# Performance work log

Measured on AMD Instinct MI355X. Metric: run time of the kernel, lower is better.

Reference implementation:

```python
import jax, jax.numpy as jnp
import numpy as np

DIM = 1024; VOCAB = 32000; HEADS = 16; HEAD_DIM = DIM // HEADS
SEG = 128; NPT = 16; WIDTH = 128
THETA = 0.1; ETA = 0.9; ALPHA = 0.01; EPS = 1e-6  # neural-memory lr / momentum / weight-decay


def l2n(x):
    return x / (jnp.linalg.norm(x, axis=-1, keepdims=True) + EPS)


def mlp(p, x):
    # 2-layer memory MLP: dim -> width -> dim, SiLU
    W1, b1, W2, b2 = p
    return jax.nn.silu(x @ W1 + b1) @ W2 + b2


def setup_inputs() -> dict:
    key = jax.random.key(0)
    ks = jax.random.split(key, 12)
    g = lambda k, s: jax.random.normal(k, s, jnp.float32) * 0.02
    z = lambda n: jnp.zeros((n,), jnp.float32)
    return {
        "x": jax.random.randint(ks[0], (2, 512), 0, VOCAB),
        "embedding": g(ks[1], (VOCAB, DIM)),
        "persistent": g(ks[2], (NPT, DIM)),
        "Wq": g(ks[3], (DIM, DIM)), "bq": z(DIM),
        "Wk": g(ks[4], (DIM, DIM)), "bk": z(DIM),
        "Wv": g(ks[5], (DIM, DIM)), "bv": z(DIM),
        "attn_in_w": g(ks[6], (DIM, 3 * DIM)), "attn_in_b": z(3 * DIM),
        "attn_out_w": g(ks[7], (DIM, DIM)), "attn_out_b": z(DIM),
        "mW1": g(ks[8], (DIM, WIDTH)), "mb1": z(WIDTH),
        "mW2": g(ks[9], (WIDTH, DIM)), "mb2": z(DIM),
        "head_w": g(ks[10], (DIM, VOCAB)), "head_b": z(VOCAB),
    }


def reference(x, embedding, persistent, Wq, bq, Wk, bk, Wv, bv,
              attn_in_w, attn_in_b, attn_out_w, attn_out_b,
              mW1, mb1, mW2, mb2, head_w, head_b):
    B, N = x.shape
    x_emb = embedding[x]  # [B, N, D]
    pad = (-N) % SEG
    if pad:
        x_emb = jnp.pad(x_emb, ((0, 0), (0, pad), (0, 0)))
    S = x_emb.shape[1] // SEG
    segs = x_emb.reshape(B, S, SEG, DIM).transpose(1, 0, 2, 3)  # [S, B, L, D]

    T = NPT + 2 * SEG  # persistent + retrieved memory + segment tokens
    causal = jnp.triu(jnp.ones((T, T), bool), 1)

    def mha(xc):  # [B, T, D] -> [B, T, D], torch nn.MultiheadAttention math
        q, k, v = jnp.split(xc @ attn_in_w + attn_in_b, 3, axis=-1)
        split = lambda t: t.reshape(B, T, HEADS, HEAD_DIM).transpose(0, 2, 1, 3)
        q, k, v = split(q), split(k), split(v)
        scores = jnp.einsum('bhqd,bhkd->bhqk', q, k) / np.sqrt(HEAD_DIM).astype(np.float32)
        scores = jnp.where(causal, -jnp.inf, scores)
        out = jnp.einsum('bhqk,bhkd->bhqd', jax.nn.softmax(scores, axis=-1), v)
        return out.transpose(0, 2, 1, 3).reshape(B, T, DIM) @ attn_out_w + attn_out_b

    # per-sample memory params (leading B axis) + zero momentum
    params0 = tuple(jnp.broadcast_to(w, (B,) + w.shape) for w in (mW1, mb1, mW2, mb2))
    mom0 = tuple(jnp.zeros_like(p) for p in params0)

    def mem_loss(p, k, v):
        e = mlp(p, k) - v
        return jnp.sum(e * e)

    def tok_step(carry, tok):  # tok: [B, D] -- one test-time gradient step on memory
        p, m = carry
        k = jax.lax.stop_gradient(l2n(tok @ Wk + bk))  # stop_grad_k=True
        v = tok @ Wv + bv                               # stop_grad_v=False
        grads = jax.vmap(jax.grad(mem_loss))(p, k, v)
        m = jax.tree.map(lambda mm, g: ETA * mm - THETA * g, m, grads)
        p = jax.tree.map(lambda pp, mm: (1.0 - ALPHA) * pp + mm, p, m)
        return (p, m), None

    retrieve = jax.vmap(mlp)  # vmap over per-sample memory params

    def seg_step(carry, segment):  # segment: [B, L, D]
        p, m = carry
        h = retrieve(p, l2n(segment @ Wq + bq))
        combined = jnp.concatenate(
            [jnp.broadcast_to(persistent, (B, NPT, DIM)), h, segment], axis=1)
        seg_out = mha(combined)[:, -SEG:, :]
        (p, m), _ = jax.lax.scan(tok_step, (p, m), seg_out.transpose(1, 0, 2))
        mem_out = retrieve(p, l2n(seg_out @ Wq + bq))
        return (p, m), seg_out * mem_out

    _, outs = jax.lax.scan(seg_step, (params0, mom0), segs)  # outs: [S, B, L, D]
    full = outs.transpose(1, 0, 2, 3).reshape(B, S * SEG, DIM)[:, :N, :]
    return full @ head_w + head_b
```

## Files before the change

### kernel.cpp

```cpp
#include <hip/hip_runtime.h>
#include <math.h>

#define D_    1024
#define B_    2
#define N_    512
#define SEG_  128
#define NSEG_ 4
#define NPT_  16
#define T_    272
#define NH_   16
#define HD_   64
#define W_    128
#define V_    32000

#define THETA_ 0.1f
#define ETA_   0.9f
#define PDEC_  0.99f
#define EPSN_  1e-6f
#define NB2_  32
#define FSTR_ 32

typedef __bf16 bf16x8 __attribute__((ext_vector_type(8)));
typedef float  f32x4  __attribute__((ext_vector_type(4)));

static const size_t XEMB = 0;
static const size_t OUTS = XEMB + (size_t)B_*N_*D_;
static const size_t PW1  = OUTS + (size_t)B_*N_*D_;
static const size_t PB1  = PW1  + (size_t)B_*D_*W_;
static const size_t PW2T = PB1  + (size_t)B_*W_;
static const size_t PB2  = PW2T + (size_t)B_*D_*W_;
static const size_t MOM  = PB2  + (size_t)B_*D_;
static const size_t MW1  = MOM;
static const size_t MB1  = MW1  + (size_t)B_*D_*W_;
static const size_t MW2T = MB1  + (size_t)B_*W_;
static const size_t MB2  = MW2T + (size_t)B_*D_*W_;
static const size_t MOMSZ = (size_t)B_*(D_*W_ + W_ + D_*W_ + D_);
static const size_t Q1   = MOM  + MOMSZ;
static const size_t AH   = Q1   + (size_t)B_*SEG_*D_;
static const size_t HBUF = AH   + (size_t)B_*SEG_*W_;
static const size_t COMB = HBUF + (size_t)B_*SEG_*D_;
static const size_t QKV  = COMB + (size_t)B_*T_*D_;
static const size_t ATTN = QKV  + (size_t)B_*T_*3*D_;
static const size_t SEGO = ATTN + (size_t)B_*SEG_*D_;
static const size_t KM   = SEGO + (size_t)B_*SEG_*D_;
static const size_t VM   = KM   + (size_t)B_*SEG_*D_;
static const size_t MEMO = VM   + (size_t)B_*SEG_*D_;
static const size_t WSEND = MEMO + (size_t)B_*SEG_*D_;

static const size_t AQ1K  = QKV;
static const size_t AQ1KM = AQ1K  + 32768;
static const size_t AGRAM = AQ1KM + 32768;
static const size_t ADZ1  = AGRAM + 32768;
static const size_t AA1H  = ADZ1  + 32768;
static const size_t AEH   = AA1H  + 32768;
static const size_t AEXR  = AEH + (size_t)B_*SEG_*D_;
static const size_t AEXEE = AEXR + 16384;
static const size_t COEF  = WSEND;
static const size_t ZEROB = COEF + 512;
static const size_t CBAR  = ZEROB + 128;

__device__ __forceinline__ float sigf(float x) { return 1.f/(1.f+expf(-x)); }

__device__ __forceinline__ void gstore(float* p, float v) {
  __hip_atomic_store(p, v, __ATOMIC_RELAXED, __HIP_MEMORY_SCOPE_AGENT);
}
__device__ __forceinline__ float gload(const float* p) {
  return __hip_atomic_load(p, __ATOMIC_RELAXED, __HIP_MEMORY_SCOPE_AGENT);
}

__device__ __forceinline__ void bsplit(float a, short& h, short& l) {
  unsigned u = __builtin_bit_cast(unsigned, a);
  unsigned hb = (u + 0x7fffu + ((u >> 16) & 1u)) >> 16;
  h = (short)hb;
  float hf = __builtin_bit_cast(float, hb << 16);
  float r = a - hf;
  unsigned ur = __builtin_bit_cast(unsigned, r);
  unsigned lb = (ur + 0x7fffu + ((ur >> 16) & 1u)) >> 16;
  l = (short)lb;
}

template<int BT, int SILU>
__global__ __launch_bounds__(256) void k_gemm(
    const float* __restrict__ A, const float* __restrict__ Bm,
    const float* __restrict__ bias, float* __restrict__ C,
    int M, int N, int K, long sA, long sB, long sC, long sBias)
{
  __shared__ float As[16][68];
  __shared__ float Bs[16][68];
  int bz = blockIdx.z;
  A += bz*sA; Bm += bz*sB; C += bz*sC; bias += bz*sBias;
  int n0 = blockIdx.x*64, m0 = blockIdx.y*64;
  int tid = threadIdx.x;
  int tx = tid & 15, ty = tid >> 4;
  int r  = tid >> 2;
  int kq = (tid & 3) * 4;
  float acc[4][4] = {};
  for (int k0 = 0; k0 < K; k0 += 16) {
    {
      int row = m0 + r;
      float4 v = make_float4(0.f,0.f,0.f,0.f);
      if (row < M) v = *(const float4*)(A + (long)row*K + k0 + kq);
      As[kq+0][r]=v.x; As[kq+1][r]=v.y; As[kq+2][r]=v.z; As[kq+3][r]=v.w;
    }
    if (BT) {
      int row = n0 + r;
      float4 v = *(const float4*)(Bm + (long)row*K + k0 + kq);
      Bs[kq+0][r]=v.x; Bs[kq+1][r]=v.y; Bs[kq+2][r]=v.z; Bs[kq+3][r]=v.w;
    } else {
      int c = tid & 63, r4 = tid >> 6;
      #pragma unroll
      for (int p = 0; p < 4; p++) {
        int kk = r4 + p*4;
        Bs[kk][c] = Bm[(long)(k0+kk)*N + n0 + c];
      }
    }
    __syncthreads();
    #pragma unroll
    for (int kk = 0; kk < 16; kk++) {
      float av[4], bv[4];
      #pragma unroll
      for (int i=0;i<4;i++) av[i] = As[kk][ty*4+i];
      #pragma unroll
      for (int j=0;j<4;j++) bv[j] = Bs[kk][tx*4+j];
      #pragma unroll
      for (int i=0;i<4;i++)
        #pragma unroll
        for (int j=0;j<4;j++)
          acc[i][j] = fmaf(av[i], bv[j], acc[i][j]);
    }
    __syncthreads();
  }
  #pragma unroll
  for (int i=0;i<4;i++) {
    int row = m0 + ty*4 + i;
    if (row >= M) continue;
    #pragma unroll
    for (int j=0;j<4;j++) {
      int col = n0 + tx*4 + j;
      float v = acc[i][j] + bias[col];
      if (SILU) v = v * sigf(v);
      C[(long)row*N + col] = v;
    }
  }
}

__global__ __launch_bounds__(256) void k_gemm2(
    const float* __restrict__ A, const float* __restrict__ B1,
    const float* __restrict__ B2, float* __restrict__ C1, float* __restrict__ C2,
    int K, long sA, long sB, long sC)
{
  __shared__ float As[16][68];
  __shared__ float B1s[16][68];
  __shared__ float B2s[16][68];
  int bz = blockIdx.z;
  A += bz*sA; B1 += bz*sB; B2 += bz*sB; C1 += bz*sC; C2 += bz*sC;
  int n0 = blockIdx.x*64, m0 = blockIdx.y*64;
  int tid = threadIdx.x;
  int tx = tid & 15, ty = tid >> 4;
  int r  = tid >> 2;
  int kq = (tid & 3) * 4;
  float acc1[4][4] = {}, acc2[4][4] = {};
  for (int k0 = 0; k0 < K; k0 += 16) {
    {
      float4 v = *(const float4*)(A + (long)(m0+r)*K + k0 + kq);
      As[kq+0][r]=v.x; As[kq+1][r]=v.y; As[kq+2][r]=v.z; As[kq+3][r]=v.w;
    }
    {
      int c = tid & 63, r4 = tid >> 6;
      #pragma unroll
      for (int p = 0; p < 4; p++) {
        int kk = r4 + p*4;
        B1s[kk][c] = B1[(long)(k0+kk)*W_ + n0 + c];
        B2s[kk][c] = B2[(long)(k0+kk)*W_ + n0 + c];
      }
    }
    __syncthreads();
    #pragma unroll
    for (int kk = 0; kk < 16; kk++) {
      float av[4], b1v[4], b2v[4];
      #pragma unroll
      for (int i=0;i<4;i++) av[i] = As[kk][ty*4+i];
      #pragma unroll
      for (int j=0;j<4;j++) { b1v[j] = B1s[kk][tx*4+j]; b2v[j] = B2s[kk][tx*4+j]; }
      #pragma unroll
      for (int i=0;i<4;i++)
        #pragma unroll
        for (int j=0;j<4;j++) {
          acc1[i][j] = fmaf(av[i], b1v[j], acc1[i][j]);
          acc2[i][j] = fmaf(av[i], b2v[j], acc2[i][j]);
        }
    }
    __syncthreads();
  }
  #pragma unroll
  for (int i=0;i<4;i++) {
    int row = m0 + ty*4 + i;
    #pragma unroll
    for (int j=0;j<4;j++) {
      int col = n0 + tx*4 + j;
      C1[(long)row*W_ + col] = acc1[i][j];
      C2[(long)row*W_ + col] = acc2[i][j];
    }
  }
}

__global__ __launch_bounds__(256) void k_gemm_mfma(
    const float* __restrict__ A, const float* __restrict__ Bm,
    const float* __restrict__ bias, float* __restrict__ C,
    int M, int N, int K, long sA, long sB, long sC, long sBias)
{
  __shared__ short Ah[128][48];
  __shared__ short Al[128][48];
  __shared__ short Bh[32][132];
  __shared__ short Bl[32][132];
  int bz = blockIdx.z;
  A += bz*sA; Bm += bz*sB; C += bz*sC; bias += bz*sBias;
  int n0 = blockIdx.x*128, m0 = blockIdx.y*128;
  int tid = threadIdx.x;
  int wave = tid >> 6, lane = tid & 63;
  int wm = (wave >> 1) * 64, wn = (wave & 1) * 64;
  int lrow = lane & 15, lk = (lane >> 4) * 8;
  int arow0 = min(m0 + (tid >> 1), M-1);
  f32x4 acc[4][4] = {};
  for (int k0 = 0; k0 < K; k0 += 32) {
    __syncthreads();
    {
      int r = tid >> 1, kq = (tid & 1) * 16;
      const float* ap = A + (long)arow0*K + k0 + kq;
      #pragma unroll
      for (int q = 0; q < 16; q += 4) {
        float4 v = *(const float4*)(ap + q);
        short h0,l0,h1,l1,h2,l2,h3,l3;
        bsplit(v.x,h0,l0); bsplit(v.y,h1,l1); bsplit(v.z,h2,l2); bsplit(v.w,h3,l3);
        *(short4*)&Ah[r][kq+q] = make_short4(h0,h1,h2,h3);
        *(short4*)&Al[r][kq+q] = make_short4(l0,l1,l2,l3);
      }
    }
    {
      int kr = tid >> 3, nq = (tid & 7) * 16;
      const float* bp = Bm + (long)(k0 + kr)*N + n0 + nq;
      #pragma unroll
      for (int q = 0; q < 16; q += 4) {
        float4 v = *(const float4*)(bp + q);
        short h0,l0,h1,l1,h2,l2,h3,l3;
        bsplit(v.x,h0,l0); bsplit(v.y,h1,l1); bsplit(v.z,h2,l2); bsplit(v.w,h3,l3);
        *(short4*)&Bh[kr][nq+q] = make_short4(h0,h1,h2,h3);
        *(short4*)&Bl[kr][nq+q] = make_short4(l0,l1,l2,l3);
      }
    }
    __syncthreads();
    bf16x8 bh[4], bl[4];
    #pragma unroll
    for (int nf = 0; nf < 4; nf++) {
      int col = wn + nf*16 + lrow;
      #pragma unroll
      for (int j = 0; j < 8; j++) {
        bh[nf][j] = __builtin_bit_cast(__bf16, Bh[lk+j][col]);
        bl[nf][j] = __builtin_bit_cast(__bf16, Bl[lk+j][col]);
      }
    }
    #pragma unroll
    for (int mf = 0; mf < 4; mf++) {
      int ar2 = wm + mf*16 + lrow;
      bf16x8 ah = *(const bf16x8*)&Ah[ar2][lk];
      bf16x8 al = *(const bf16x8*)&Al[ar2][lk];
      #pragma unroll
      for (int nf = 0; nf < 4; nf++) {
        acc[mf][nf] = __builtin_amdgcn_mfma_f32_16x16x32_bf16(ah, bh[nf], acc[mf][nf], 0, 0, 0);
        acc[mf][nf] = __builtin_amdgcn_mfma_f32_16x16x32_bf16(ah, bl[nf], acc[mf][nf], 0, 0, 0);
        acc[mf][nf] = __builtin_amdgcn_mfma_f32_16x16x32_bf16(al, bh[nf], acc[mf][nf], 0, 0, 0);
      }
    }
  }
  #pragma unroll
  for (int mf = 0; mf < 4; mf++) {
    #pragma unroll
    for (int nf = 0; nf < 4; nf++) {
      int col = n0 + wn + nf*16 + lrow;
      float bv = bias[col];
      #pragma unroll
      for (int j = 0; j < 4; j++) {
        int row = m0 + wm + mf*16 + (lane >> 4)*4 + j;
        if (row < M) C[(long)row*N + col] = acc[mf][nf][j] + bv;
      }
    }
  }
}

__global__ __launch_bounds__(256) void k_qkv_mfma(
    const float* __restrict__ pers, const float* __restrict__ hbuf,
    const float* __restrict__ xemb, int s,
    const float* __restrict__ Bm, const float* __restrict__ bias,
    float* __restrict__ C)
{
  __shared__ short Ah[128][48];
  __shared__ short Al[128][48];
  __shared__ short Bh[32][132];
  __shared__ short Bl[32][132];
  const int M = B_*T_, N = 3*D_, K = D_;
  int n0 = blockIdx.x*128, m0 = blockIdx.y*128;
  int tid = threadIdx.x;
  int wave = tid >> 6, lane = tid & 63;
  int wm = (wave >> 1) * 64, wn = (wave & 1) * 64;
  int lrow = lane & 15, lk = (lane >> 4) * 8;
  int grow = min(m0 + (tid >> 1), M-1);
  int b = grow >= T_ ? 1 : 0;
  int rt = grow - b*T_;
  const float* asrc;
  if (rt < NPT_)            asrc = pers + (long)rt*D_;
  else if (rt < NPT_+SEG_)  asrc = hbuf + ((long)b*SEG_ + (rt-NPT_))*D_;
  else                      asrc = xemb + ((long)b*N_ + s*SEG_ + (rt-NPT_-SEG_))*D_;
  f32x4 acc[4][4] = {};
  for (int k0 = 0; k0 < K; k0 += 32) {
    __syncthreads();
    {
      int r = tid >> 1, kq = (tid & 1) * 16;
      const float* ap = asrc + k0 + kq;
      #pragma unroll
      for (int q = 0; q < 16; q += 4) {
        float4 v = *(const float4*)(ap + q);
        short h0,l0,h1,l1,h2,l2,h3,l3;
        bsplit(v.x,h0,l0); bsplit(v.y,h1,l1); bsplit(v.z,h2,l2); bsplit(v.w,h3,l3);
        *(short4*)&Ah[r][kq+q] = make_short4(h0,h1,h2,h3);
        *(short4*)&Al[r][kq+q] = make_short4(l0,l1,l2,l3);
      }
    }
    {
      int kr = tid >> 3, nq = (tid & 7) * 16;
      const float* bp = Bm + (long)(k0 + kr)*N + n0 + nq;
      #pragma unroll
      for (int q = 0; q < 16; q += 4) {
        float4 v = *(const float4*)(bp + q);
        short h0,l0,h1,l1,h2,l2,h3,l3;
        bsplit(v.x,h0,l0); bsplit(v.y,h1,l1); bsplit(v.z,h2,l2); bsplit(v.w,h3,l3);
        *(short4*)&Bh[kr][nq+q] = make_short4(h0,h1,h2,h3);
        *(short4*)&Bl[kr][nq+q] = make_short4(l0,l1,l2,l3);
      }
    }
    __syncthreads();
    bf16x8 bh[4], bl[4];
    #pragma unroll
    for (int nf = 0; nf < 4; nf++) {
      int col = wn + nf*16 + lrow;
      #pragma unroll
      for (int j = 0; j < 8; j++) {
        bh[nf][j] = __builtin_bit_cast(__bf16, Bh[lk+j][col]);
        bl[nf][j] = __builtin_bit_cast(__bf16, Bl[lk+j][col]);
      }
    }
    #pragma unroll
    for (int mf = 0; mf < 4; mf++) {
      int ar2 = wm + mf*16 + lrow;
      bf16x8 ah = *(const bf16x8*)&Ah[ar2][lk];
      bf16x8 al = *(const bf16x8*)&Al[ar2][lk];
      #pragma unroll
      for (int nf = 0; nf < 4; nf++) {
        acc[mf][nf] = __builtin_amdgcn_mfma_f32_16x16x32_bf16(ah, bh[nf], acc[mf][nf], 0, 0, 0);
        acc[mf][nf] = __builtin_amdgcn_mfma_f32_16x16x32_bf16(ah, bl[nf], acc[mf][nf], 0, 0, 0);
        acc[mf][nf] = __builtin_amdgcn_mfma_f32_16x16x32_bf16(al, bh[nf], acc[mf][nf], 0, 0, 0);
      }
    }
  }
  #pragma unroll
  for (int mf = 0; mf < 4; mf++) {
    #pragma unroll
    for (int nf = 0; nf < 4; nf++) {
      int col = n0 + wn + nf*16 + lrow;
// ... 155 lines not shown
      #pragma unroll
      for (int nf = 0; nf < 4; nf++) {
        acc[mf][nf] = __builtin_amdgcn_mfma_f32_16x16x32_bf16(ah, bh[nf], acc[mf][nf], 0, 0, 0);
        acc[mf][nf] = __builtin_amdgcn_mfma_f32_16x16x32_bf16(ah, bl[nf], acc[mf][nf], 0, 0, 0);
        acc[mf][nf] = __builtin_amdgcn_mfma_f32_16x16x32_bf16(al, bh[nf], acc[mf][nf], 0, 0, 0);
      }
    }
  }
  #pragma unroll
  for (int mf = 0; mf < 4; mf++) {
    #pragma unroll
    for (int nf = 0; nf < 4; nf++) {
      int col = n0 + wn + nf*16 + lrow;
      float bv = bias[col];
      #pragma unroll
      for (int j = 0; j < 4; j++) {
        int row = m0 + wm + mf*16 + (lane >> 4)*4 + j;
        C[(long)row*N + col] = acc[mf][nf][j] + bv;
      }
    }
  }
}

__global__ void k_embed(const int* __restrict__ x, const float* __restrict__ emb,
                        float* __restrict__ xe)
{
  int row = blockIdx.x, tid = threadIdx.x;
  int idx = x[row];
  float4 v = *(const float4*)(emb + (long)idx*D_ + tid*4);
  *(float4*)(xe + (long)row*D_ + tid*4) = v;
}

#define PER_ 263296L
__global__ void k_init(const float* __restrict__ mW1in, const float* __restrict__ mb1in,
                       const float* __restrict__ mW2in, const float* __restrict__ mb2in,
                       float* __restrict__ pW1, float* __restrict__ pb1,
                       float* __restrict__ pW2T, float* __restrict__ pb2)
{
  long g = (long)blockIdx.x*256 + threadIdx.x;
  if (g >= 2*PER_) return;
  int b = (int)(g / PER_);
  long rr = g % PER_;
  if (rr < 131072)       pW1[(long)b*131072 + rr] = mW1in[rr];
  else if (rr < 131200)  pb1[b*W_ + (rr-131072)] = mb1in[rr-131072];
  else if (rr < 262272) { long l = rr-131200; int j=(int)(l>>7), h=(int)(l&127);
                          pW2T[(long)b*131072 + l] = mW2in[(long)h*D_ + j]; }
  else                   pb2[b*D_ + (rr-262272)] = mb2in[rr-262272];
}

__global__ void k_coef(float* __restrict__ c)
{
  if (blockIdx.x == 0 && threadIdx.x == 0) {
    c[0] = 1.f; c[128] = 1.f;
    float A = 1.f, eta_d = 1.f;
    for (int d = 1; d < 128; d++) {
      eta_d *= ETA_;
      A = PDEC_*A + eta_d;
      c[d] = A;
      c[128 + d] = eta_d;
    }
    c[256] = 1.f;
    float bp = 1.f;
    for (int t = 1; t <= 128; t++) { bp *= PDEC_; c[256 + t] = bp; }
  }
}

__global__ __launch_bounds__(256) void k_l2n(float* __restrict__ X)
{
  long row = blockIdx.x;
  float* p = X + row*D_;
  int tid = threadIdx.x;
  float4 v = *(float4*)(p + tid*4);
  float ss = v.x*v.x + v.y*v.y + v.z*v.z + v.w*v.w;
  for (int o=32;o;o>>=1) ss += __shfl_xor(ss,o);
  __shared__ float wsum[4];
  if ((tid&63)==0) wsum[tid>>6] = ss;
  __syncthreads();
  float tot = wsum[0]+wsum[1]+wsum[2]+wsum[3];
  float sc = 1.f/(sqrtf(tot)+EPSN_);
  v.x*=sc; v.y*=sc; v.z*=sc; v.w*=sc;
  *(float4*)(p + tid*4) = v;
}

__global__ __launch_bounds__(256) void k_attn(const float* __restrict__ qkv,
                                              float* __restrict__ outp)
{
  __shared__ float sQ[16][68];
  __shared__ float sKV[64][68];
  __shared__ float sS[16][273];
  int qt = blockIdx.x, head = blockIdx.y, b = blockIdx.z;
  int tid = threadIdx.x;
  const float* base = qkv + (long)b*T_*3*D_;
  int qoff = head*HD_, koff = D_ + head*HD_, voff = 2*D_ + head*HD_;
  int qrow0 = NPT_ + SEG_ + qt*16;
  {
    int rr = tid>>4, c4 = (tid&15)*4;
    float4 v = *(const float4*)(base + (long)(qrow0+rr)*3*D_ + qoff + c4);
    sQ[rr][c4]=v.x; sQ[rr][c4+1]=v.y; sQ[rr][c4+2]=v.z; sQ[rr][c4+3]=v.w;
  }
  __syncthreads();
  for (int j0 = 0; j0 < T_; j0 += 64) {
    int chunk = min(64, T_ - j0);
    {
      int jj = tid>>2, cq = (tid&3)*16;
      if (jj < chunk) {
        #pragma unroll
        for (int q4=0;q4<4;q4++) {
          float4 v = *(const float4*)(base + (long)(j0+jj)*3*D_ + koff + cq + q4*4);
          sKV[jj][cq+q4*4]=v.x; sKV[jj][cq+q4*4+1]=v.y; sKV[jj][cq+q4*4+2]=v.z; sKV[jj][cq+q4*4+3]=v.w;
        }
      }
    }
    __syncthreads();
    int rr = tid>>4, jj0 = tid&15;
    #pragma unroll
    for (int p=0;p<4;p++) {
      int jj = jj0 + p*16;
      if (jj < chunk) {
        float s = 0.f;
        #pragma unroll 8
        for (int c=0;c<HD_;c++) s = fmaf(sQ[rr][c], sKV[jj][c], s);
        s *= 0.125f;
        int jg = j0 + jj, qg = qrow0 + rr;
        if (jg > qg) s = -3.0e38f;
        sS[rr][jg] = s;
      }
    }
    __syncthreads();
  }
  {
    int rr = tid>>4, l16 = tid&15;
    float m = -3.4e38f;
    for (int j=l16; j<T_; j+=16) m = fmaxf(m, sS[rr][j]);
    for (int o=8;o;o>>=1) m = fmaxf(m, __shfl_xor(m,o));
    float sum = 0.f;
    for (int j=l16; j<T_; j+=16) { float e = expf(sS[rr][j]-m); sS[rr][j] = e; sum += e; }
    for (int o=8;o;o>>=1) sum += __shfl_xor(sum,o);
    float inv = 1.f/sum;
    for (int j=l16; j<T_; j+=16) sS[rr][j] *= inv;
  }
  __syncthreads();
  float acc[4] = {0.f,0.f,0.f,0.f};
  int rr = tid>>4, c4 = (tid&15)*4;
  for (int j0 = 0; j0 < T_; j0 += 64) {
    int chunk = min(64, T_ - j0);
    {
      int jj = tid>>2, cq = (tid&3)*16;
      if (jj < chunk) {
        #pragma unroll
        for (int q4=0;q4<4;q4++) {
          float4 v = *(const float4*)(base + (long)(j0+jj)*3*D_ + voff + cq + q4*4);
          sKV[jj][cq+q4*4]=v.x; sKV[jj][cq+q4*4+1]=v.y; sKV[jj][cq+q4*4+2]=v.z; sKV[jj][cq+q4*4+3]=v.w;
        }
      }
    }
    __syncthreads();
    for (int jj=0; jj<chunk; jj++) {
      float p = sS[rr][j0+jj];
      #pragma unroll
      for (int i=0;i<4;i++) acc[i] = fmaf(p, sKV[jj][c4+i], acc[i]);
    }
    __syncthreads();
  }
  float4 o4 = make_float4(acc[0],acc[1],acc[2],acc[3]);
  *(float4*)(outp + ((long)(b*SEG_) + qt*16 + rr)*D_ + head*HD_ + c4) = o4;
}

__device__ __forceinline__ void gbar(int* flags, int blk, int gen)
{
  asm volatile("s_waitcnt vmcnt(0) lgkmcnt(0)" ::: "memory");
  __syncthreads();
  if (threadIdx.x == 0)
    __hip_atomic_store(flags + blk*FSTR_, gen, __ATOMIC_RELAXED, __HIP_MEMORY_SCOPE_AGENT);
  if (threadIdx.x < NB2_) {
    while (__hip_atomic_load(flags + threadIdx.x*FSTR_, __ATOMIC_RELAXED,
                             __HIP_MEMORY_SCOPE_AGENT) < gen)
      __builtin_amdgcn_s_sleep(1);
  }
  __syncthreads();
}

__global__ __launch_bounds__(256) void k_scan(
  const float* __restrict__ pW2T, const float* __restrict__ mW2T,
  float* __restrict__ pb1, float* __restrict__ mb1,
  float* __restrict__ pb2, float* __restrict__ mb2,
  const float* __restrict__ Vm,
  const float* __restrict__ q1k, const float* __restrict__ q1km,
  const float* __restrict__ G,
  float* __restrict__ dz1o, float* __restrict__ a1o, float* __restrict__ eo,
  float* __restrict__ exR, float* __restrict__ exEE,
  const float* __restrict__ coef, int* __restrict__ barbase, int seg)
{
  __shared__ float sDZ[128][129];
  __shared__ float sA1[128][129];
  __shared__ float sEh[128][33];
  __shared__ float sB1[128], sMB1[128], sZ1[128], sR[128];
  __shared__ float sB2[32], sMB2[32];
  __shared__ float sAt[128];
  __shared__ float sBp[129];
  __shared__ float sGc[128];
  __shared__ float sS[128];
  __shared__ float sEEc[128];
  __shared__ float sP[2][128];

  int b = blockIdx.y, blk = blockIdx.x, tid = threadIdx.x;
  int j0 = blk*32;
  int* flags = barbase + b*(NB2_*FSTR_);
  int gbase = seg*200;
  const float* W0 = pW2T + (long)b*131072;
  const float* Wm = mW2T + (long)b*131072;

  int jD = tid >> 3, lD = tid & 7;
  float rD0[16], rDm[16];
  #pragma unroll
  for (int k = 0; k < 16; k++) {
    rD0[k] = W0[(long)(j0+jD)*128 + lD + 8*k];
    rDm[k] = Wm[(long)(j0+jD)*128 + lD + 8*k];
  }
  int hE = tid >> 1, halfE = tid & 1;
  float rE0[16], rEm[16];
  #pragma unroll
  for (int q = 0; q < 16; q++) {
    rE0[q] = W0[(long)(j0 + halfE*16 + q)*128 + hE];
    rEm[q] = Wm[(long)(j0 + halfE*16 + q)*128 + hE];
  }

  int hB = tid & 127, halfB = tid >> 7;
  if (tid < 128) { sAt[tid] = coef[tid]; sB1[tid] = pb1[b*W_+tid]; sMB1[tid] = mb1[b*W_+tid]; }
  else if (tid < 160) { int j = tid-128; sB2[j] = pb2[b*D_+j0+j]; sMB2[j] = mb2[b*D_+j0+j]; }
  for (int i = tid; i < 129; i += 256) sBp[i] = coef[256+i];
  __syncthreads();

  for (int t = 0; t < SEG_; ++t) {
    int par = t & 1;
    float bp = sBp[t];
    float ca = (t>0) ? ETA_*sAt[t-1] : 0.f;
    int th = t >> 1;

    float rq1k = 0.f, rq1km = 0.f;
    if (tid < 128) {
      rq1k  = q1k [((long)b*SEG_+t)*W_ + tid];
      rq1km = q1km[((long)b*SEG_+t)*W_ + tid];
      if (t > 0) {
        float mm = ETA_*sMB1[tid] - THETA_*sDZ[t-1][tid];
        sMB1[tid] = mm; sB1[tid] = PDEC_*sB1[tid] + mm;
      }
      if (tid < t) sGc[tid] = sAt[t-1-tid]*G[((long)b*SEG_+t)*SEG_ + tid];
    } else if (tid < 160) {
      int j = tid-128;
      if (t > 0) {
        float mm = ETA_*sMB2[j] - 2.f*THETA_*sEh[t-1][j];
        sMB2[j] = mm; sB2[j] = PDEC_*sB2[j] + mm;
      }
    }
    __syncthreads();

    {
      int u0 = halfB ? th : 0, u1 = halfB ? t : th;
      float acc = 0.f;
      for (int u = u0; u < u1; ++u) acc = fmaf(sGc[u], sDZ[u][hB], acc);
      sP[halfB][hB] = acc;
    }
    __syncthreads();
    if (tid < 128) {
      float z1 = bp*rq1k + ca*rq1km + sB1[tid] - THETA_*(sP[0][tid] + sP[1][tid]);
      sZ1[tid] = z1;
      sA1[t][tid] = z1 * sigf(z1);
    }
    __syncthreads();

    {
      int u = tid & 127, half = tid >> 7;
      float acc = 0.f;
      if (u < t) {
        #pragma unroll 8
        for (int h = half*64; h < half*64 + 64; ++h)
          acc = fmaf(sA1[u][h], sA1[t][h], acc);
      }
      sP[half][u] = acc;
    }
    __syncthreads();
    if (tid < t) sS[tid] = -2.f*THETA_*sAt[t-1-tid]*(sP[0][tid] + sP[1][tid]);
    __syncthreads();

    {
      float g = 0.f, gm = 0.f;
      #pragma unroll
      for (int k = 0; k < 16; k++) {
        float a = sA1[t][lD + 8*k];
        g  = fmaf(rD0[k], a, g);
        gm = fmaf(rDm[k], a, gm);
      }
      float corr = 0.f;
      for (int u = lD; u < t; u += 8) corr = fmaf(sS[u], sEh[u][jD], corr);
      float tot = bp*g + ca*gm + corr;
      tot += __shfl_xor(tot,4); tot += __shfl_xor(tot,2); tot += __shfl_xor(tot,1);
      if (lD == 0) sEh[t][jD] = tot + sB2[jD] - Vm[((long)b*SEG_+t)*D_ + j0+jD];
    }
    __syncthreads();

    {
      float racc = 0.f;
      #pragma unroll
      for (int q = 0; q < 16; ++q) {
        float w = bp*rE0[q] + ca*rEm[q];
        racc = fmaf(w, sEh[t][halfE*16 + q], racc);
      }
      racc += __shfl_xor(racc,1);
      if (halfE == 0) gstore(&exR[(((long)par*B_ + b)*NB2_ + blk)*W_ + hE], racc);
      if (hE < t) {
        float eacc = 0.f;
        #pragma unroll
        for (int q = 0; q < 16; ++q)
          eacc = fmaf(sEh[hE][halfE*16 + q], sEh[t][halfE*16 + q], eacc);
        eacc += __shfl_xor(eacc,1);
        if (halfE == 0) gstore(&exEE[(((long)par*B_ + b)*NB2_ + blk)*W_ + hE], eacc);
      }
    }
    gbar(flags, blk, gbase + t + 1);

    {
      float racc = 0.f;
      #pragma unroll
      for (int k = 0; k < 16; ++k)
        racc += gload(&exR[(((long)par*B_ + b)*NB2_ + halfE*16 + k)*W_ + hE]);
      racc += __shfl_xor(racc,1);
      if (halfE == 0) sR[hE] = racc;
      if (hE < t) {
        float eacc = 0.f;
        #pragma unroll
        for (int k = 0; k < 16; ++k)
          eacc += gload(&exEE[(((long)par*B_ + b)*NB2_ + halfE*16 + k)*W_ + hE]);
        eacc += __shfl_xor(eacc,1);
        if (halfE == 0) sEEc[hE] = -2.f*THETA_*sAt[t-1-hE]*eacc;
      }
    }
    __syncthreads();
    {
      int u0 = halfB ? th : 0, u1 = halfB ? t : th;
      float acc = 0.f;
      for (int u = u0; u < u1; ++u) acc = fmaf(sEEc[u], sA1[u][hB], acc);
      sP[halfB][hB] = acc;
    }
    __syncthreads();
    if (tid < 128) {
      float macc = sP[0][tid] + sP[1][tid];
      float z = sZ1[tid], sg = sigf(z);
      sDZ[t][tid] = 2.f*(sR[tid] + macc)*sg*(1.f + z*(1.f - sg));
    }
    __syncthreads();
  }

  if (tid < 128) {
    if (blk == 0) {
      float mm = ETA_*sMB1[tid] - THETA_*sDZ[127][tid];
      mb1[b*W_ + tid] = mm;
      pb1[b*W_ + tid] = PDEC_*sB1[tid] + mm;
    }
  } else if (tid < 160) {
    int j = tid-128;
    float mm = ETA_*sMB2[j] - 2.f*THETA_*sEh[127][j];
    mb2[b*D_ + j0+j] = mm;
    pb2[b*D_ + j0+j] = PDEC_*sB2[j] + mm;
  }
  for (int i = tid; i < 128*4; i += 256) {
    int t2 = i >> 2, hh = (i & 3) + blk*4;
    dz1o[((long)b*SEG_+t2)*W_ + hh] = sDZ[t2][hh];
    a1o [((long)b*SEG_+t2)*W_ + hh] = sA1[t2][hh];
  }
  for (int i = tid; i < 128*32; i += 256) {
    int t2 = i >> 5, jj = i & 31;
    eo[((long)b*SEG_+t2)*D_ + j0+jj] = sEh[t2][jj];
  }
}

__global__ __launch_bounds__(256) void k_recon(
  float* __restrict__ pW1, float* __restrict__ mW1,
  float* __restrict__ pW2T, float* __restrict__ mW2T,
  const float* __restrict__ KMp, const float* __restrict__ Eh,
  const float* __restrict__ DZ1, const float* __restrict__ A1h,
  const float* __restrict__ coef)
{
  __shared__ float s1[16][33];
  __shared__ float s2[16][65];
  __shared__ float sCA[128], sCE[128];
  int dt = blockIdx.x, ht = blockIdx.y, kb = blockIdx.z;
  int kind = kb >> 1, b = kb & 1;
  int tid = threadIdx.x;
  int d0 = dt*32, hb = ht*64;
  const float* in1 = (kind ? Eh : KMp) + (long)b*SEG_*D_;
  const float* in2 = (kind ? A1h : DZ1) + (long)b*SEG_*W_;
  float* Pb = (kind ? pW2T : pW1) + (long)b*131072;
  float* Mb = (kind ? mW2T : mW1) + (long)b*131072;
  float f = kind ? -2.f*THETA_ : -THETA_;
  if (tid < 128) {
    sCA[tid] = f*coef[127 - tid];
    sCE[tid] = f*coef[128 + 127 - tid];
  }
  __syncthreads();
  int dd = tid >> 3, le = tid & 7;
  float accP[8] = {}, accM[8] = {};
  for (int u0 = 0; u0 < 128; u0 += 16) {
    for (int i = tid; i < 16*32; i += 256) {
      int uu = i >> 5, d2 = i & 31;
      s1[uu][d2] = in1[(long)(u0+uu)*D_ + d0 + d2];
    }
    for (int i = tid; i < 16*64; i += 256) {
      int uu = i >> 6, hl = i & 63;
      s2[uu][hl] = in2[(long)(u0+uu)*W_ + hb + hl];
    }
    __syncthreads();
    #pragma unroll
    for (int uu = 0; uu < 16; uu++) {
      float a = s1[uu][dd];
      float cAu = sCA[u0+uu], cEu = sCE[u0+uu];
      #pragma unroll
      for (int k = 0; k < 8; k++) {
        float v = a * s2[uu][k*8 + le];
        accP[k] = fmaf(cAu, v, accP[k]);
        accM[k] = fmaf(cEu, v, accM[k]);
      }
    }
    __syncthreads();
  }
  float b128 = coef[256 + 128];
  float eA   = ETA_*coef[127];
  float e128 = ETA_*coef[128 + 127];
  #pragma unroll
  for (int k = 0; k < 8; k++) {
    long idx = (long)(d0+dd)*W_ + hb + k*8 + le;
    float Po = Pb[idx], Mo = Mb[idx];
    Pb[idx] = b128*Po + eA*Mo + accP[k];
    Mb[idx] = e128*Mo + accM[k];
  }
}

__global__ void k_mul(const float* __restrict__ so, const float* __restrict__ mo,
                      float* __restrict__ outs, int s)
{
  int l = blockIdx.x, b = blockIdx.y, tid = threadIdx.x;
  long src = ((long)b*SEG_ + l)*D_ + tid*4;
  float4 a = *(const float4*)(so + src);
  float4 c = *(const float4*)(mo + src);
  a.x*=c.x; a.y*=c.y; a.z*=c.z; a.w*=c.w;
  *(float4*)(outs + ((long)b*N_ + s*SEG_ + l)*D_ + tid*4) = a;
}

static inline void gemm(const float* A, const float* Bm, const float* bias, float* C,
                        int M, int N, int K, long sA, long sB, long sC, long sBias,
                        int batch, int bt, int silu_, hipStream_t st)
{
  dim3 g(N/64, (M+63)/64, batch), blk(256);
  if (!bt && !silu_) k_gemm<0,0><<<g,blk,0,st>>>(A,Bm,bias,C,M,N,K,sA,sB,sC,sBias);
  else if (!bt && silu_) k_gemm<0,1><<<g,blk,0,st>>>(A,Bm,bias,C,M,N,K,sA,sB,sC,sBias);
  else k_gemm<1,0><<<g,blk,0,st>>>(A,Bm,bias,C,M,N,K,sA,sB,sC,sBias);
}

extern "C" void kernel_launch(void* const* d_in, const int* in_sizes, int n_in,
                              void* d_out, int out_size, void* d_ws, size_t ws_size,
                              hipStream_t stream)
{
  (void)in_sizes; (void)n_in; (void)out_size; (void)ws_size;
  const int*   x     = (const int*)  d_in[0];
  const float* emb   = (const float*)d_in[1];
  const float* pers  = (const float*)d_in[2];
  const float* Wq    = (const float*)d_in[3];
  const float* bq    = (const float*)d_in[4];
  const float* Wk    = (const float*)d_in[5];
  const float* bk    = (const float*)d_in[6];
  const float* Wv    = (const float*)d_in[7];
  const float* bv    = (const float*)d_in[8];
  const float* aiw   = (const float*)d_in[9];
  const float* aib   = (const float*)d_in[10];
  const float* aow   = (const float*)d_in[11];
  const float* aob   = (const float*)d_in[12];
  const float* mW1in = (const float*)d_in[13];
  const float* mb1in = (const float*)d_in[14];
  const float* mW2in = (const float*)d_in[15];
  const float* mb2in = (const float*)d_in[16];
  const float* headw = (const float*)d_in[17];
  const float* headb = (const float*)d_in[18];
  float* out = (float*)d_out;
  float* ws  = (float*)d_ws;

  hipMemsetAsync(ws + MOM, 0, MOMSZ*sizeof(float), stream);
  hipMemsetAsync(ws + ZEROB, 0, 128*sizeof(float), stream);
  hipMemsetAsync(ws + CBAR, 0, (size_t)B_*NB2_*FSTR_*sizeof(int), stream);
  k_embed<<<dim3(B_*N_), dim3(256), 0, stream>>>(x, emb, ws+XEMB);
  k_init<<<dim3((2*PER_+255)/256), dim3(256), 0, stream>>>(
      mW1in, mb1in, mW2in, mb2in, ws+PW1, ws+PB1, ws+PW2T, ws+PB2);
  k_coef<<<dim3(1), dim3(64), 0, stream>>>(ws+COEF);

  for (int s = 0; s < NSEG_; s++) {
    const float* segA = ws + XEMB + (size_t)s*SEG_*D_;
    k_gemm_mfma<<<dim3(8, 1, B_), dim3(256), 0, stream>>>(
        segA, Wq, bq, ws+Q1, SEG_, D_, D_, (long)N_*D_, 0, (long)SEG_*D_, 0);
    k_l2n<<<dim3(B_*SEG_), dim3(256), 0, stream>>>(ws+Q1);
    gemm(ws+Q1, ws+PW1, ws+PB1, ws+AH, SEG_, W_, D_, (long)SEG_*D_, (long)D_*W_, (long)SEG_*W_, W_, B_, 0, 1, stream);
    gemm(ws+AH, ws+PW2T, ws+PB2, ws+HBUF, SEG_, D_, W_, (long)SEG_*W_, (long)D_*W_, (long)SEG_*D_, D_, B_, 1, 0, stream);
    k_qkv_mfma<<<dim3(3*D_/128, (B_*T_+127)/128), dim3(256), 0, stream>>>(
        pers, ws+HBUF, ws+XEMB, s, aiw, aib, ws+QKV);
    k_attn<<<dim3(8, NH_, B_), dim3(256), 0, stream>>>(ws+QKV, ws+ATTN);
    k_gemm_mfma<<<dim3(D_/128, 2, 1), dim3(256), 0, stream>>>(
        ws+ATTN, aow, aob, ws+SEGO, B_*SEG_, D_, D_, 0, 0, 0, 0);
    k_gemmkvq_m<<<dim3(24, 2), dim3(256), 0, stream>>>(
        ws+SEGO, Wk, bk, Wv, bv, Wq, bq, ws+KM, ws+VM, ws+Q1);
    k_l2n<<<dim3(B_*SEG_), dim3(256), 0, stream>>>(ws+KM);
    k_l2n<<<dim3(B_*SEG_), dim3(256), 0, stream>>>(ws+Q1);
    k_gemm2<<<dim3(2, 2, B_), dim3(256), 0, stream>>>(
        ws+KM, ws+PW1, ws+MW1, ws+AQ1K, ws+AQ1KM,
        D_, (long)SEG_*D_, (long)D_*W_, (long)SEG_*W_);
    gemm(ws+KM, ws+KM,  ws+ZEROB, ws+AGRAM, SEG_, SEG_, D_, (long)SEG_*D_, (long)SEG_*D_, (long)SEG_*SEG_, 0, B_, 1, 0, stream);
    k_scan<<<dim3(NB2_, B_), dim3(256), 0, stream>>>(
        ws+PW2T, ws+MW2T, ws+PB1, ws+MB1, ws+PB2, ws+MB2, ws+VM,
        ws+AQ1K, ws+AQ1KM, ws+AGRAM,
        ws+ADZ1, ws+AA1H, ws+AEH,
        ws+AEXR, ws+AEXEE,
        ws+COEF, (int*)(ws+CBAR), s);
    k_recon<<<dim3(32, 2, 4), dim3(256), 0, stream>>>(
        ws+PW1, ws+MW1, ws+PW2T, ws+MW2T,
        ws+KM, ws+AEH, ws+ADZ1, ws+AA1H, ws+COEF);
    gemm(ws+Q1, ws+PW1, ws+PB1, ws+AH, SEG_, W_, D_, (long)SEG_*D_, (long)D_*W_, (long)SEG_*W_, W_, B_, 0, 1, stream);
    gemm(ws+AH, ws+PW2T, ws+PB2, ws+MEMO, SEG_, D_, W_, (long)SEG_*W_, (long)D_*W_, (long)SEG_*D_, D_, B_, 1, 0, stream);
    k_mul<<<dim3(SEG_, B_), dim3(256), 0, stream>>>(ws+SEGO, ws+MEMO, ws+OUTS, s);
  }
  k_head_mfma<<<dim3(V_/128, (B_*N_)/128), dim3(256), 0, stream>>>(
      ws+OUTS, headw, headb, out, B_*N_, V_, D_);
}
```

Measured before the change: 7.650 ms.

## Replace scalar FP32 memory-MLP GEMMs with split-bf16 MFMA kernel and fuse epilogues

Replaces the scalar 64x64-tile FP32 GEMM used for the memory MLP retrieval and the key Gram matrix with a templated split-bf16 MFMA kernel (128x128 tiles), adding SiLU and optional elementwise-multiply epilogues. The final retrieval GEMM now multiplies by the segment output and writes straight into the output buffer, which removes the separate k_mul kernel. The two l2-normalisations are merged into one launch. The scan kernel's two-half partial sums are also collapsed back into single-thread loops, which removes a sync per step but halves the parallelism of those reductions. The small GEMMs now launch as few as two blocks, and precision depends on the hi/lo bf16 split.

Result: no change. 7.678 ms (+0.4%).

```diff
diff --git a/kernel.cpp b/kernel.cpp
--- a/kernel.cpp
+++ b/kernel.cpp
@@ -79,67 +79,104 @@
   l = (short)lb;
 }
 
-template<int BT, int SILU>
-__global__ __launch_bounds__(256) void k_gemm(
+template<int BT, int SILU, int MUL>
+__global__ __launch_bounds__(256) void k_mf(
     const float* __restrict__ A, const float* __restrict__ Bm,
     const float* __restrict__ bias, float* __restrict__ C,
-    int M, int N, int K, long sA, long sB, long sC, long sBias)
-{
-  __shared__ float As[16][68];
-  __shared__ float Bs[16][68];
+    const float* __restrict__ aux,
+    int M, int N, int K, long sA, long sB, long sC, long sBias, long sAux)
+{
+  __shared__ short Ah[128][48];
+  __shared__ short Al[128][48];
+  __shared__ short Bh[32][132];
+  __shared__ short Bl[32][132];
   int bz = blockIdx.z;
   A += bz*sA; Bm += bz*sB; C += bz*sC; bias += bz*sBias;
-  int n0 = blockIdx.x*64, m0 = blockIdx.y*64;
+  if (MUL) aux += bz*sAux;
+  int n0 = blockIdx.x*128, m0 = blockIdx.y*128;
   int tid = threadIdx.x;
-  int tx = tid & 15, ty = tid >> 4;
-  int r  = tid >> 2;
-  int kq = (tid & 3) * 4;
-  float acc[4][4] = {};
-  for (int k0 = 0; k0 < K; k0 += 16) {
-    {
-      int row = m0 + r;
-      float4 v = make_float4(0.f,0.f,0.f,0.f);
-      if (row < M) v = *(const float4*)(A + (long)row*K + k0 + kq);
-      As[kq+0][r]=v.x; As[kq+1][r]=v.y; As[kq+2][r]=v.z; As[kq+3][r]=v.w;
+  int wave = tid >> 6, lane = tid & 63;
+  int wm = (wave >> 1) * 64, wn = (wave & 1) * 64;
+  int lrow = lane & 15, lk = (lane >> 4) * 8;
+  int arow0 = min(m0 + (tid >> 1), M-1);
+  f32x4 acc[4][4] = {};
+  for (int k0 = 0; k0 < K; k0 += 32) {
+    __syncthreads();
+    {
+      int r = tid >> 1, kq = (tid & 1) * 16;
+      const float* ap = A + (long)arow0*K + k0 + kq;
+      #pragma unroll
+      for (int q = 0; q < 16; q += 4) {
+        float4 v = *(const float4*)(ap + q);
+        short h0,l0,h1,l1,h2,l2,h3,l3;
+        bsplit(v.x,h0,l0); bsplit(v.y,h1,l1); bsplit(v.z,h2,l2); bsplit(v.w,h3,l3);
+        *(short4*)&Ah[r][kq+q] = make_short4(h0,h1,h2,h3);
+        *(short4*)&Al[r][kq+q] = make_short4(l0,l1,l2,l3);
+      }
     }
     if (BT) {
-      int row = n0 + r;
-      float4 v = *(const float4*)(Bm + (long)row*K + k0 + kq);
-      Bs[kq+0][r]=v.x; Bs[kq+1][r]=v.y; Bs[kq+2][r]=v.z; Bs[kq+3][r]=v.w;
+      int nn = tid >> 1, kq2 = (tid & 1) * 16;
+      const float* bp = Bm + (long)(n0+nn)*K + k0 + kq2;
+      #pragma unroll
+      for (int q = 0; q < 16; q += 4) {
+        float4 v = *(const float4*)(bp + q);
+        short h0,l0,h1,l1,h2,l2,h3,l3;
+        bsplit(v.x,h0,l0); bsplit(v.y,h1,l1); bsplit(v.z,h2,l2); bsplit(v.w,h3,l3);
+        Bh[kq2+q+0][nn]=h0; Bh[kq2+q+1][nn]=h1; Bh[kq2+q+2][nn]=h2; Bh[kq2+q+3][nn]=h3;
+        Bl[kq2+q+0][nn]=l0; Bl[kq2+q+1][nn]=l1; Bl[kq2+q+2][nn]=l2; Bl[kq2+q+3][nn]=l3;
+      }
     } else {
-      int c = tid & 63, r4 = tid >> 6;
-      #pragma unroll
-      for (int p = 0; p < 4; p++) {
-        int kk = r4 + p*4;
-        Bs[kk][c] = Bm[(long)(k0+kk)*N + n0 + c];
-      }
-    }
-    __syncthreads();
-    #pragma unroll
-    for (int kk = 0; kk < 16; kk++) {
-      float av[4], bv[4];
-      #pragma unroll
-      for (int i=0;i<4;i++) av[i] = As[kk][ty*4+i];
-      #pragma unroll
-      for (int j=0;j<4;j++) bv[j] = Bs[kk][tx*4+j];
-      #pragma unroll
-      for (int i=0;i<4;i++)
-        #pragma unroll
-        for (int j=0;j<4;j++)
-          acc[i][j] = fmaf(av[i], bv[j], acc[i][j]);
-    }
-    __syncthreads();
+      int kr = tid >> 3, nq = (tid & 7) * 16;
+      const float* bp = Bm + (long)(k0 + kr)*N + n0 + nq;
+      #pragma unroll
+      for (int q = 0; q < 16; q += 4) {
+        float4 v = *(const float4*)(bp + q);
+        short h0,l0,h1,l1,h2,l2,h3,l3;
+        bsplit(v.x,h0,l0); bsplit(v.y,h1,l1); bsplit(v.z,h2,l2); bsplit(v.w,h3,l3);
+        *(short4*)&Bh[kr][nq+q] = make_short4(h0,h1,h2,h3);
+        *(short4*)&Bl[kr][nq+q] = make_short4(l0,l1,l2,l3);
+      }
+    }
+    __syncthreads();
+    bf16x8 bh[4], bl[4];
+    #pragma unroll
+    for (int nf = 0; nf < 4; nf++) {
+      int col = wn + nf*16 + lrow;
+      #pragma unroll
+      for (int j = 0; j < 8; j++) {
+        bh[nf][j] = __builtin_bit_cast(__bf16, Bh[lk+j][col]);
+        bl[nf][j] = __builtin_bit_cast(__bf16, Bl[lk+j][col]);
+      }
+    }
+    #pragma unroll
+    for (int mf = 0; mf < 4; mf++) {
+      int ar2 = wm + mf*16 + lrow;
+      bf16x8 ah = *(const bf16x8*)&Ah[ar2][lk];
+      bf16x8 al = *(const bf16x8*)&Al[ar2][lk];
+      #pragma unroll
+      for (int nf = 0; nf < 4; nf++) {
+        acc[mf][nf] = __builtin_amdgcn_mfma_f32_16x16x32_bf16(ah, bh[nf], acc[mf][nf], 0, 0, 0);
+        acc[mf][nf] = __builtin_amdgcn_mfma_f32_16x16x32_bf16(ah, bl[nf], acc[mf][nf], 0, 0, 0);
+        acc[mf][nf] = __builtin_amdgcn_mfma_f32_16x16x32_bf16(al, bh[nf], acc[mf][nf], 0, 0, 0);
+      }
+    }
   }
   #pragma unroll
-  for (int i=0;i<4;i++) {
-    int row = m0 + ty*4 + i;
-    if (row >= M) continue;
-    #pragma unroll
-    for (int j=0;j<4;j++) {
-      int col = n0 + tx*4 + j;
-      float v = acc[i][j] + bias[col];
-      if (SILU) v = v * sigf(v);
-      C[(long)row*N + col] = v;
+  for (int mf = 0; mf < 4; mf++) {
+    #pragma unroll
+    for (int nf = 0; nf < 4; nf++) {
+      int col = n0 + wn + nf*16 + lrow;
+      float bv = bias[col];
+      #pragma unroll
+      for (int j = 0; j < 4; j++) {
+        int row = m0 + wm + mf*16 + (lane >> 4)*4 + j;
+        if (row < M) {
+          float v = acc[mf][nf][j] + bv;
+          if (SILU) v = v * sigf(v);
+          if (MUL)  v *= aux[(long)row*N + col];
+          C[(long)row*N + col] = v;
+        }
+      }
     }
   }
 }
@@ -200,89 +237,6 @@
       int col = n0 + tx*4 + j;
       C1[(long)row*W_ + col] = acc1[i][j];
       C2[(long)row*W_ + col] = acc2[i][j];
-    }
-  }
-}
-
-__global__ __launch_bounds__(256) void k_gemm_mfma(
-    const float* __restrict__ A, const float* __restrict__ Bm,
-    const float* __restrict__ bias, float* __restrict__ C,
-    int M, int N, int K, long sA, long sB, long sC, long sBias)
-{
-  __shared__ short Ah[128][48];
-  __shared__ short Al[128][48];
-  __shared__ short Bh[32][132];
-  __shared__ short Bl[32][132];
-  int bz = blockIdx.z;
-  A += bz*sA; Bm += bz*sB; C += bz*sC; bias += bz*sBias;
-  int n0 = blockIdx.x*128, m0 = blockIdx.y*128;
-  int tid = threadIdx.x;
-  int wave = tid >> 6, lane = tid & 63;
-  int wm = (wave >> 1) * 64, wn = (wave & 1) * 64;
-  int lrow = lane & 15, lk = (lane >> 4) * 8;
-  int arow0 = min(m0 + (tid >> 1), M-1);
-  f32x4 acc[4][4] = {};
-  for (int k0 = 0; k0 < K; k0 += 32) {
-    __syncthreads();
-    {
-      int r = tid >> 1, kq = (tid & 1) * 16;
-      const float* ap = A + (long)arow0*K + k0 + kq;
-      #pragma unroll
-      for (int q = 0; q < 16; q += 4) {
-        float4 v = *(const float4*)(ap + q);
-        short h0,l0,h1,l1,h2,l2,h3,l3;
-        bsplit(v.x,h0,l0); bsplit(v.y,h1,l1); bsplit(v.z,h2,l2); bsplit(v.w,h3,l3);
-        *(short4*)&Ah[r][kq+q] = make_short4(h0,h1,h2,h3);
-        *(short4*)&Al[r][kq+q] = make_short4(l0,l1,l2,l3);
-      }
-    }
-    {
-      int kr = tid >> 3, nq = (tid & 7) * 16;
-      const float* bp = Bm + (long)(k0 + kr)*N + n0 + nq;
-      #pragma unroll
-      for (int q = 0; q < 16; q += 4) {
-        float4 v = *(const float4*)(bp + q);
-        short h0,l0,h1,l1,h2,l2,h3,l3;
-        bsplit(v.x,h0,l0); bsplit(v.y,h1,l1); bsplit(v.z,h2,l2); bsplit(v.w,h3,l3);
-        *(short4*)&Bh[kr][nq+q] = make_short4(h0,h1,h2,h3);
-        *(short4*)&Bl[kr][nq+q] = make_short4(l0,l1,l2,l3);
-      }
-    }
-    __syncthreads();
-    bf16x8 bh[4], bl[4];
-    #pragma unroll
-    for (int nf = 0; nf < 4; nf++) {
-      int col = wn + nf*16 + lrow;
-      #pragma unroll
-      for (int j = 0; j < 8; j++) {
-        bh[nf][j] = __builtin_bit_cast(__bf16, Bh[lk+j][col]);
-        bl[nf][j] = __builtin_bit_cast(__bf16, Bl[lk+j][col]);
-      }
-    }
-    #pragma unroll
-    for (int mf = 0; mf < 4; mf++) {
-      int ar2 = wm + mf*16 + lrow;
-      bf16x8 ah = *(const bf16x8*)&Ah[ar2][lk];
-      bf16x8 al = *(const bf16x8*)&Al[ar2][lk];
-      #pragma unroll
-      for (int nf = 0; nf < 4; nf++) {
-        acc[mf][nf] = __builtin_amdgcn_mfma_f32_16x16x32_bf16(ah, bh[nf], acc[mf][nf], 0, 0, 0);
-        acc[mf][nf] = __builtin_amdgcn_mfma_f32_16x16x32_bf16(ah, bl[nf], acc[mf][nf], 0, 0, 0);
-        acc[mf][nf] = __builtin_amdgcn_mfma_f32_16x16x32_bf16(al, bh[nf], acc[mf][nf], 0, 0, 0);
-      }
-    }
-  }
-  #pragma unroll
-  for (int mf = 0; mf < 4; mf++) {
-    #pragma unroll
-    for (int nf = 0; nf < 4; nf++) {
-      int col = n0 + wn + nf*16 + lrow;
-      float bv = bias[col];
-      #pragma unroll
-      for (int j = 0; j < 4; j++) {
-        int row = m0 + wm + mf*16 + (lane >> 4)*4 + j;
-        if (row < M) C[(long)row*N + col] = acc[mf][nf][j] + bv;
-      }
     }
   }
 }
@@ -604,6 +558,23 @@
   *(float4*)(p + tid*4) = v;
 }
 
+__global__ __launch_bounds__(256) void k_l2n2(float* __restrict__ X1, float* __restrict__ X2, int R)
+{
+  int row = blockIdx.x;
+  float* p = (row < R ? X1 + (long)row*D_ : X2 + (long)(row-R)*D_);
+  int tid = threadIdx.x;
+  float4 v = *(float4*)(p + tid*4);
+  float ss = v.x*v.x + v.y*v.y + v.z*v.z + v.w*v.w;
+  for (int o=32;o;o>>=1) ss += __shfl_xor(ss,o);
+  __shared__ float wsum[4];
+  if ((tid&63)==0) wsum[tid>>6] = ss;
+  __syncthreads();
+  float tot = wsum[0]+wsum[1]+wsum[2]+wsum[3];
+  float sc = 1.f/(sqrtf(tot)+EPSN_);
+  v.x*=sc; v.y*=sc; v.z*=sc; v.w*=sc;
+  *(float4*)(p + tid*4) = v;
+}
+
 __global__ __launch_bounds__(256) void k_attn(const float* __restrict__ qkv,
                                               float* __restrict__ outp)
 {
@@ -723,7 +694,6 @@
   __shared__ float sGc[128];
   __shared__ float sS[128];
   __shared__ float sEEc[128];
-  __shared__ float sP[2][128];
 
   int b = blockIdx.y, blk = blockIdx.x, tid = threadIdx.x;
   int j0 = blk*32;
@@ -747,7 +717,6 @@
     rEm[q] = Wm[(long)(j0 + halfE*16 + q)*128 + hE];
   }
 
-  int hB = tid & 127, halfB = tid >> 7;
   if (tid < 128) { sAt[tid] = coef[tid]; sB1[tid] = pb1[b*W_+tid]; sMB1[tid] = mb1[b*W_+tid]; }
   else if (tid < 160) { int j = tid-128; sB2[j] = pb2[b*D_+j0+j]; sMB2[j] = mb2[b*D_+j0+j]; }
   for (int i = tid; i < 129; i += 256) sBp[i] = coef[256+i];
@@ -757,7 +726,6 @@
     int par = t & 1;
     float bp = sBp[t];
     float ca = (t>0) ? ETA_*sAt[t-1] : 0.f;
-    int th = t >> 1;
 
     float rq1k = 0.f, rq1km = 0.f;
     if (tid < 128) {
@@ -777,32 +745,21 @@
     }
     __syncthreads();
 
-    {
-      int u0 = halfB ? th : 0, u1 = halfB ? t : th;
+    if (tid < 128) {
       float acc = 0.f;
-      for (int u = u0; u < u1; ++u) acc = fmaf(sGc[u], sDZ[u][hB], acc);
-      sP[halfB][hB] = acc;
-    }
-    __syncthreads();
-    if (tid < 128) {
-      float z1 = bp*rq1k + ca*rq1km + sB1[tid] - THETA_*(sP[0][tid] + sP[1][tid]);
+      for (int u = 0; u < t; ++u) acc = fmaf(sGc[u], sDZ[u][tid], acc);
+      float z1 = bp*rq1k + ca*rq1km + sB1[tid] - THETA_*acc;
       sZ1[tid] = z1;
       sA1[t][tid] = z1 * sigf(z1);
     }
     __syncthreads();
 
-    {
-      int u = tid & 127, half = tid >> 7;
+    if (tid < t) {
       float acc = 0.f;
-      if (u < t) {
-        #pragma unroll 8
-        for (int h = half*64; h < half*64 + 64; ++h)
-          acc = fmaf(sA1[u][h], sA1[t][h], acc);
-      }
-      sP[half][u] = acc;
-    }
-    __syncthreads();
-    if (tid < t) sS[tid] = -2.f*THETA_*sAt[t-1-tid]*(sP[0][tid] + sP[1][tid]);
+      #pragma unroll 8
+      for (int h = 0; h < 128; ++h) acc = fmaf(sA1[tid][h], sA1[t][h], acc);
+      sS[tid] = -2.f*THETA_*sAt[t-1-tid]*acc;
+    }
     __syncthreads();
 
     {
@@ -858,15 +815,9 @@
       }
     }
     __syncthreads();
-    {
-      int u0 = halfB ? th : 0, u1 = halfB ? t : th;
-      float acc = 0.f;
-      for (int u = u0; u < u1; ++u) acc = fmaf(sEEc[u], sA1[u][hB], acc);
-      sP[halfB][hB] = acc;
-    }
-    __syncthreads();
     if (tid < 128) {
-      float macc = sP[0][tid] + sP[1][tid];
+      float macc = 0.f;
+      for (int u = 0; u < t; ++u) macc = fmaf(sEEc[u], sA1[u][tid], macc);
       float z = sZ1[tid], sg = sigf(z);
       sDZ[t][tid] = 2.f*(sR[tid] + macc)*sg*(1.f + z*(1.f - sg));
     }
@@ -955,27 +906,6 @@
     Pb[idx] = b128*Po + eA*Mo + accP[k];
     Mb[idx] = e128*Mo + accM[k];
   }
-}
-
-__global__ void k_mul(const float* __restrict__ so, const float* __restrict__ mo,
-                      float* __restrict__ outs, int s)
-{
-  int l = blockIdx.x, b = blockIdx.y, tid = threadIdx.x;
-  long src = ((long)b*SEG_ + l)*D_ + tid*4;
-  float4 a = *(const float4*)(so + src);
-  float4 c = *(const float4*)(mo + src);
-  a.x*=c.x; a.y*=c.y; a.z*=c.z; a.w*=c.w;
-  *(float4*)(outs + ((long)b*N_ + s*SEG_ + l)*D_ + tid*4) = a;
-}
-
-static inline void gemm(const float* A, const float* Bm, const float* bias, float* C,
-                        int M, int N, int K, long sA, long sB, long sC, long sBias,
-                        int batch, int bt, int silu_, hipStream_t st)
-{
-  dim3 g(N/64, (M+63)/64, batch), blk(256);
-  if (!bt && !silu_) k_gemm<0,0><<<g,blk,0,st>>>(A,Bm,bias,C,M,N,K,sA,sB,sC,sBias);
-  else if (!bt && silu_) k_gemm<0,1><<<g,blk,0,st>>>(A,Bm,bias,C,M,N,K,sA,sB,sC,sBias);
-  else k_gemm<1,0><<<g,blk,0,st>>>(A,Bm,bias,C,M,N,K,sA,sB,sC,sBias);
 }
 
 extern "C" void kernel_launch(void* const* d_in, const int* in_sizes, int n_in,
@@ -1015,24 +945,29 @@
 
   for (int s = 0; s < NSEG_; s++) {
     const float* segA = ws + XEMB + (size_t)s*SEG_*D_;
-    k_gemm_mfma<<<dim3(8, 1, B_), dim3(256), 0, stream>>>(
-        segA, Wq, bq, ws+Q1, SEG_, D_, D_, (long)N_*D_, 0, (long)SEG_*D_, 0);
+    k_mf<0,0,0><<<dim3(8,1,B_), dim3(256), 0, stream>>>(
+        segA, Wq, bq, ws+Q1, nullptr, SEG_, D_, D_, (long)N_*D_, 0, (long)SEG_*D_, 0, 0);
     k_l2n<<<dim3(B_*SEG_), dim3(256), 0, stream>>>(ws+Q1);
-    gemm(ws+Q1, ws+PW1, ws+PB1, ws+AH, SEG_, W_, D_, (long)SEG_*D_, (long)D_*W_, (long)SEG_*W_, W_, B_, 0, 1, stream);
-    gemm(ws+AH, ws+PW2T, ws+PB2, ws+HBUF, SEG_, D_, W_, (long)SEG_*W_, (long)D_*W_, (long)SEG_*D_, D_, B_, 1, 0, stream);
+    k_mf<0,1,0><<<dim3(1,1,B_), dim3(256), 0, stream>>>(
+        ws+Q1, ws+PW1, ws+PB1, ws+AH, nullptr, SEG_, W_, D_,
+        (long)SEG_*D_, (long)D_*W_, (long)SEG_*W_, W_, 0);
+    k_mf<1,0,0><<<dim3(8,1,B_), dim3(256), 0, stream>>>(
+        ws+AH, ws+PW2T, ws+PB2, ws+HBUF, nullptr, SEG_, D_, W_,
+        (long)SEG_*W_, (long)D_*W_, (long)SEG_*D_, D_, 0);
     k_qkv_mfma<<<dim3(3*D_/128, (B_*T_+127)/128), dim3(256), 0, stream>>>(
         pers, ws+HBUF, ws+XEMB, s, aiw, aib, ws+QKV);
     k_attn<<<dim3(8, NH_, B_), dim3(256), 0, stream>>>(ws+QKV, ws+ATTN);
-    k_gemm_mfma<<<dim3(D_/128, 2, 1), dim3(256), 0, stream>>>(
-        ws+ATTN, aow, aob, ws+SEGO, B_*SEG_, D_, D_, 0, 0, 0, 0);
+    k_mf<0,0,0><<<dim3(D_/128, 2, 1), dim3(256), 0, stream>>>(
+        ws+ATTN, aow, aob, ws+SEGO, nullptr, B_*SEG_, D_, D_, 0, 0, 0, 0, 0);
     k_gemmkvq_m<<<dim3(24, 2), dim3(256), 0, stream>>>(
         ws+SEGO, Wk, bk, Wv, bv, Wq, bq, ws+KM, ws+VM, ws+Q1);
-    k_l2n<<<dim3(B_*SEG_), dim3(256), 0, stream>>>(ws+KM);
-    k_l2n<<<dim3(B_*SEG_), dim3(256), 0, stream>>>(ws+Q1);
+    k_l2n2<<<dim3(2*B_*SEG_), dim3(256), 0, stream>>>(ws+KM, ws+Q1, B_*SEG_);
     k_gemm2<<<dim3(2, 2, B_), dim3(256), 0, stream>>>(
         ws+KM, ws+PW1, ws+MW1, ws+AQ1K, ws+AQ1KM,
         D_, (long)SEG_*D_, (long)D_*W_, (long)SEG_*W_);
-    gemm(ws+KM, ws+KM,  ws+ZEROB, ws+AGRAM, SEG_, SEG_, D_, (long)SEG_*D_, (long)SEG_*D_, (long)SEG_*SEG_, 0, B_, 1, 0, stream);
+    k_mf<1,0,0><<<dim3(1,1,B_), dim3(256), 0, stream>>>(
+        ws+KM, ws+KM, ws+ZEROB, ws+AGRAM, nullptr, SEG_, SEG_, D_,
+        (long)SEG_*D_, (long)SEG_*D_, (long)SEG_*SEG_, 0, 0);
     k_scan<<<dim3(NB2_, B_), dim3(256), 0, stream>>>(
         ws+PW2T, ws+MW2T, ws+PB1, ws+MB1, ws+PB2, ws+MB2, ws+VM,
         ws+AQ1K, ws+AQ1KM, ws+AGRAM,
@@ -1042,9 +977,12 @@
     k_recon<<<dim3(32, 2, 4), dim3(256), 0, stream>>>(
         ws+PW1, ws+MW1, ws+PW2T, ws+MW2T,
         ws+KM, ws+AEH, ws+ADZ1, ws+AA1H, ws+COEF);
-    gemm(ws+Q1, ws+PW1, ws+PB1, ws+AH, SEG_, W_, D_, (long)SEG_*D_, (long)D_*W_, (long)SEG_*W_, W_, B_, 0, 1, stream);
-    gemm(ws+AH, ws+PW2T, ws+PB2, ws+MEMO, SEG_, D_, W_, (long)SEG_*W_, (long)D_*W_, (long)SEG_*D_, D_, B_, 1, 0, stream);
-    k_mul<<<dim3(SEG_, B_), dim3(256), 0, stream>>>(ws+SEGO, ws+MEMO, ws+OUTS, s);
+    k_mf<0,1,0><<<dim3(1,1,B_), dim3(256), 0, stream>>>(
+        ws+Q1, ws+PW1, ws+PB1, ws+AH, nullptr, SEG_, W_, D_,
+        (long)SEG_*D_, (long)D_*W_, (long)SEG_*W_, W_, 0);
+    k_mf<1,0,1><<<dim3(8,1,B_), dim3(256), 0, stream>>>(
+        ws+AH, ws+PW2T, ws+PB2, ws+OUTS + (size_t)s*SEG_*D_, ws+SEGO,
+        SEG_, D_, W_, (long)SEG_*W_, (long)D_*W_, (long)N_*D_, D_, (long)SEG_*D_);
   }
   k_head_mfma<<<dim3(V_/128, (B_*N_)/128), dim3(256), 0, stream>>>(
       ws+OUTS, headw, headb, out, B_*N_, V_, D_);
```
